# Kernel tuning notes

Hardware: AMD Instinct MI355X
Metric: run time of the kernel (lower is better)

Reference implementation:

```python
import jax, jax.numpy as jnp
import numpy as np

B, S, H, HD, WIN, KS = 2, 2048, 8, 64, 64, 2048
D = H * HD          # slotsize = nheads * headsize = 512
SUB = 1 + 2 * WIN   # window length = 129
LN_EPS = 1e-3       # Keras LayerNormalization default epsilon


def setup_inputs() -> dict:
    key = jax.random.key(0)
    ks = jax.random.split(key, 5)
    s = 0.02
    return {
        "values": jax.random.normal(ks[0], (B, S, D), jnp.float32),
        "W_kqv": jax.random.normal(ks[1], (D, 3 * D), jnp.float32) * s,
        "b_kqv": jnp.zeros((3 * D,), jnp.float32),
        "ln_gamma": jnp.ones((D,), jnp.float32),
        "ln_beta": jnp.zeros((D,), jnp.float32),
        "W_kernel": jax.random.normal(ks[2], (D, KS), jnp.float32) * s,
        "b_kernel": jnp.zeros((KS,), jnp.float32),
        "W_proj": jax.random.normal(ks[3], (KS, D), jnp.float32) * s,
        "b_proj": jnp.zeros((D,), jnp.float32),
    }


def _layernorm(x, g, b):
    mu = jnp.mean(x, axis=-1, keepdims=True)
    var = jnp.var(x, axis=-1, keepdims=True)
    return (x - mu) * jax.lax.rsqrt(var + LN_EPS) * g + b


def reference(values, W_kqv, b_kqv, ln_gamma, ln_beta, W_kernel, b_kernel, W_proj, b_proj):
    # fused qkv projection: [B,S,3D]
    kqv = values @ W_kqv + b_kqv
    k, q, v = jnp.split(kqv, 3, axis=2)
    # shared layernorm applied to q and k (over full D)
    q = _layernorm(q, ln_gamma, ln_beta)
    k = _layernorm(k, ln_gamma, ln_beta)
    kh = k.reshape(B, S, H, HD)
    qh = q.reshape(B, S, H, HD)
    vh = v.reshape(B, S, H, HD)
    starts = jnp.clip(jnp.arange(S) - WIN, 0, S - SUB)
    idx = starts[:, None] + jnp.arange(SUB)          # [S, SUB]
    kw = kh[:, idx]                                  # [B,S,SUB,H,HD]
    vw = vh[:, idx]                                  # [B,S,SUB,H,HD]
    scores = jnp.einsum('bshd,bswhd->bshw', qh, kw) / np.float32(np.sqrt(HD))
    attn = jax.nn.softmax(scores, axis=-1)           # [B,S,H,SUB]
    ctx = jnp.einsum('bshw,bswhd->bshd', attn, vw).reshape(B, S, D)
    # residual MLP (dropout rate 0 -> identity)
    x = jax.nn.relu(ctx @ W_kernel + b_kernel)
    x = x @ W_proj + b_proj
    return x + v  # residual is the value projection, per the original code
```

## Files before the change

### kernel.cpp

```cpp
#include <hip/hip_runtime.h>
#include <hip/hip_bf16.h>

#define B_ 2
#define S_ 2048
#define H_ 8
#define HD_ 64
#define WIN_ 64
#define SUB_ 129
#define D_ 512
#define KS_ 2048
#define M_ 4096
#define LN_EPS 1e-3f

typedef unsigned short u16;
typedef short bf16x8 __attribute__((ext_vector_type(8)));
typedef _Float16 f16x8 __attribute__((ext_vector_type(8)));
typedef float f32x4 __attribute__((ext_vector_type(4)));

__device__ inline u16 f2bf(float x) {
  unsigned int u = __float_as_uint(x);
  return (u16)((u + 0x7fffu + ((u >> 16) & 1u)) >> 16);
}

__device__ inline void gll16(const u16* g, u16* l) {
  __builtin_amdgcn_global_load_lds(
      (const __attribute__((address_space(1))) void*)g,
      (__attribute__((address_space(3))) void*)l, 16, 0, 0);
}

template <int EPI>
__global__ __launch_bounds__(256) void mfma_gemm(
    const u16* __restrict__ A, const u16* __restrict__ Bt,
    const float* __restrict__ bias, const float* __restrict__ extra,
    void* __restrict__ Cout, int K, int lda, int ldb, int ldc, int eld,
    int TN) {
  __shared__ __align__(16) u16 As[2][8192];
  __shared__ __align__(16) u16 Bs[2][8192];

  const int tid = threadIdx.x;
  const int wv = tid >> 6;
  const int ln = tid & 63;

  const int id = blockIdx.x;
  const int xcd = id & 7;
  const int sub = id >> 3;
  const int tn = sub % TN;
  const int msub = sub / TN;
  const int row0 = (xcd * 4 + msub) << 7;
  const int col0 = tn << 7;

  const int lrow = ln >> 3;
  const int lchunk = (ln & 7) ^ lrow;
  const u16* ag = A + (size_t)(row0 + 32 * wv + lrow) * lda + lchunk * 8;
  const u16* bg = Bt + (size_t)(col0 + 32 * wv + lrow) * ldb + lchunk * 8;
  const int lbase = 32 * wv * 64;

  const int q = ln >> 4;
  const int r16 = ln & 15;
  const int r8 = r16 & 7;
  const int wm = (wv & 1) << 6;
  const int wn = (wv >> 1) << 6;

  f32x4 acc[4][4];
#pragma unroll
  for (int i = 0; i < 4; ++i)
#pragma unroll
    for (int j = 0; j < 4; ++j) acc[i][j] = (f32x4){0.f, 0.f, 0.f, 0.f};

#define STAGE(buf, koff)                                            \
  do {                                                              \
    const u16* a0 = ag + (koff);                                    \
    const u16* b0 = bg + (koff);                                    \
    u16* la = &As[buf][lbase];                                      \
    u16* lb = &Bs[buf][lbase];                                      \
    gll16(a0, la);                                                  \
    gll16(a0 + 8 * (size_t)lda, la + 512);                          \
    gll16(a0 + 16 * (size_t)lda, la + 1024);                        \
    gll16(a0 + 24 * (size_t)lda, la + 1536);                        \
    gll16(b0, lb);                                                  \
    gll16(b0 + 8 * (size_t)ldb, lb + 512);                          \
    gll16(b0 + 16 * (size_t)ldb, lb + 1024);                        \
    gll16(b0 + 24 * (size_t)ldb, lb + 1536);                        \
  } while (0)

  const int nk = K >> 6;
  STAGE(0, 0);

  for (int ki = 0; ki < nk; ++ki) {
    __syncthreads();
    if (ki + 1 < nk) STAGE((ki + 1) & 1, (ki + 1) << 6);

    const char* Ab = (const char*)As[ki & 1];
    const char* Bb = (const char*)Bs[ki & 1];
#pragma unroll
    for (int ks = 0; ks < 2; ++ks) {
      const int pc = ((q + 4 * ks) ^ r8) << 4;
      bf16x8 af[4], bfv[4];
#pragma unroll
      for (int mi = 0; mi < 4; ++mi)
        af[mi] = *(const bf16x8*)(Ab + (wm + 16 * mi + r16) * 128 + pc);
#pragma unroll
      for (int ni = 0; ni < 4; ++ni)
        bfv[ni] = *(const bf16x8*)(Bb + (wn + 16 * ni + r16) * 128 + pc);
#pragma unroll
      for (int mi = 0; mi < 4; ++mi)
#pragma unroll
        for (int ni = 0; ni < 4; ++ni)
          acc[mi][ni] = __builtin_amdgcn_mfma_f32_16x16x32_bf16(
              af[mi], bfv[ni], acc[mi][ni], 0, 0, 0);
    }
  }
#undef STAGE

  const int colb = col0 + wn + r16;
  float bv[4];
#pragma unroll
  for (int ni = 0; ni < 4; ++ni) bv[ni] = bias[colb + ni * 16];

#pragma unroll
  for (int mi = 0; mi < 4; ++mi) {
#pragma unroll
    for (int ni = 0; ni < 4; ++ni) {
      const int col = colb + ni * 16;
#pragma unroll
      for (int r = 0; r < 4; ++r) {
        const int row = row0 + wm + mi * 16 + (q << 2) + r;
        float v = acc[mi][ni][r] + bv[ni];
        if (EPI == 0) {
          ((float*)Cout)[(size_t)row * ldc + col] = v;
        } else if (EPI == 1) {
          ((u16*)Cout)[(size_t)row * ldc + col] = f2bf(fmaxf(v, 0.f));
        } else {
          ((float*)Cout)[(size_t)row * ldc + col] =
              v + extra[(size_t)row * eld + col];
        }
      }
    }
  }
}

__global__ __launch_bounds__(256) void cvt_kernel(const float* __restrict__ in,
                                                  u16* __restrict__ out) {
  const int i = (blockIdx.x * 256 + threadIdx.x) * 8;
  float4 a = *(const float4*)&in[i];
  float4 b = *(const float4*)&in[i + 4];
  union { u16 u[8]; uint4 v; } pk;
  pk.u[0] = f2bf(a.x); pk.u[1] = f2bf(a.y); pk.u[2] = f2bf(a.z); pk.u[3] = f2bf(a.w);
  pk.u[4] = f2bf(b.x); pk.u[5] = f2bf(b.y); pk.u[6] = f2bf(b.z); pk.u[7] = f2bf(b.w);
  *(uint4*)&out[i] = pk.v;
}

__global__ __launch_bounds__(256) void cvtT_kernel(const float* __restrict__ W,
                                                   u16* __restrict__ Wt, int K,
                                                   int N) {
  __shared__ float t[32][33];
  const int n0 = blockIdx.x << 5;
  const int k0 = blockIdx.y << 5;
  const int r = threadIdx.x >> 3;
  const int c4 = (threadIdx.x & 7) << 2;
  float4 v = *(const float4*)&W[(size_t)(k0 + r) * N + n0 + c4];
  t[r][c4 + 0] = v.x; t[r][c4 + 1] = v.y; t[r][c4 + 2] = v.z; t[r][c4 + 3] = v.w;
  __syncthreads();
  ushort4 o;
  o.x = f2bf(t[c4 + 0][r]); o.y = f2bf(t[c4 + 1][r]);
  o.z = f2bf(t[c4 + 2][r]); o.w = f2bf(t[c4 + 3][r]);
  *(ushort4*)&Wt[(size_t)(n0 + r) * K + k0 + c4] = o;
}

__global__ __launch_bounds__(128) void ln_kernel(float* __restrict__ kqv,
                                                 const float* __restrict__ gamma,
                                                 const float* __restrict__ beta) {
  const int row = blockIdx.x;
  const int bs = row >> 1;
  const int which = row & 1;
  float* p = kqv + (size_t)bs * 1536 + (which ? 512 : 0);
  const int tid = threadIdx.x;
  const int c = tid << 2;

  float4 xv = *(float4*)&p[c];
  float s = xv.x + xv.y + xv.z + xv.w;
  float ss = xv.x * xv.x + xv.y * xv.y + xv.z * xv.z + xv.w * xv.w;

#pragma unroll
  for (int off = 32; off > 0; off >>= 1) {
    s += __shfl_down(s, off);
    ss += __shfl_down(ss, off);
  }
  __shared__ float red[4];
  if ((tid & 63) == 0) {
    red[(tid >> 6) * 2 + 0] = s;
    red[(tid >> 6) * 2 + 1] = ss;
  }
  __syncthreads();
  const float tot = red[0] + red[2];
  const float tots = red[1] + red[3];
  const float mean = tot * (1.f / 512.f);
  const float var = tots * (1.f / 512.f) - mean * mean;
  const float rstd = rsqrtf(var + LN_EPS);

  float4 g = *(const float4*)&gamma[c];
  float4 bb = *(const float4*)&beta[c];
  xv.x = (xv.x - mean) * rstd * g.x + bb.x;
  xv.y = (xv.y - mean) * rstd * g.y + bb.y;
  xv.z = (xv.z - mean) * rstd * g.z + bb.z;
  xv.w = (xv.w - mean) * rstd * g.w + bb.w;
  *(float4*)&p[c] = xv;
}

__global__ __launch_bounds__(256) void attn_kernel(const float* __restrict__ kqv,
                                                   u16* __restrict__ ctx) {
  __shared__ __align__(16) u16 Ks[192 * 64];
  __shared__ __align__(16) u16 Vt[64 * 192];
  __shared__ __align__(16) u16 Ps[4 * 16 * 192];

  const int bid = blockIdx.x;
  const int tile = bid & 31;
  const int h = (bid >> 5) & 7;
  const int b = bid >> 8;
  const int t0 = tile << 6;

  int g0 = t0 - WIN_;
  if (g0 < 0) g0 = 0;
  if (g0 > S_ - SUB_) g0 = S_ - SUB_;

  const int tid = threadIdx.x;
  const size_t rowb = (size_t)(b * S_);

#pragma unroll
  for (int it = 0; it < 6; ++it) {
    const int item = tid + it * 256;
    const int key = item >> 3, c = item & 7;
    const int phys = c ^ (key & 7);
    const float* kp = &kqv[(rowb + g0 + key) * 1536 + h * 64 + c * 8];
    float4 a = *(const float4*)kp;
    float4 bb = *(const float4*)(kp + 4);
    union { u16 u[8]; uint4 v; } pk;
    pk.u[0] = f2bf(a.x); pk.u[1] = f2bf(a.y); pk.u[2] = f2bf(a.z); pk.u[3] = f2bf(a.w);
    pk.u[4] = f2bf(bb.x); pk.u[5] = f2bf(bb.y); pk.u[6] = f2bf(bb.z); pk.u[7] = f2bf(bb.w);
    *(uint4*)&Ks[key * 64 + phys * 8] = pk.v;
  }
#pragma unroll
  for (int it = 0; it < 2; ++it) {
    const int item = tid + it * 256;
    const int qq = item >> 3, c = item & 7;
    const int phys = c ^ (qq & 7);
    const float* qp = &kqv[(rowb + t0 + qq) * 1536 + 512 + h * 64 + c * 8];
    float4 a = *(const float4*)qp;
    float4 bb = *(const float4*)(qp + 4);
    union { u16 u[8]; uint4 v; } pk;
    pk.u[0] = f2bf(a.x * 0.125f); pk.u[1] = f2bf(a.y * 0.125f);
    pk.u[2] = f2bf(a.z * 0.125f); pk.u[3] = f2bf(a.w * 0.125f);
    pk.u[4] = f2bf(bb.x * 0.125f); pk.u[5] = f2bf(bb.y * 0.125f);
    pk.u[6] = f2bf(bb.z * 0.125f); pk.u[7] = f2bf(bb.w * 0.125f);
    *(uint4*)&Ps[qq * 64 + phys * 8] = pk.v;
  }
#pragma unroll
  for (int it = 0; it < 12; ++it) {
    const int item = tid + it * 256;
    const int dg = item / 192;
    const int key = item - dg * 192;
    const float* vp = &kqv[(rowb + g0 + key) * 1536 + 1024 + h * 64 + dg * 4];
    float4 v = *(const float4*)vp;
#pragma unroll
    for (int j = 0; j < 4; ++j) {
      const int d = dg * 4 + j;
      const int c = key >> 3;
      const int phys = (c & 24) | ((c ^ d) & 7);
      const float f = (j == 0) ? v.x : (j == 1) ? v.y : (j == 2) ? v.z : v.w;
      *(_Float16*)&Vt[d * 192 + phys * 8 + (key & 7)] = (_Float16)f;
    }
  }
  __syncthreads();

  const int wv = tid >> 6;
  const int ln = tid & 63;
  const int quad = ln >> 4;
  const int l15 = ln & 15;
  const int l7 = l15 & 7;
  const int qbase = wv << 4;

  bf16x8 qf[2];
#pragma unroll
  for (int ks = 0; ks < 2; ++ks) {
    const int phys = (ks * 4 + quad) ^ l7;
    qf[ks] = *(const bf16x8*)&Ps[(qbase + l15) * 64 + phys * 8];
  }

  f32x4 sacc[12];
#pragma unroll
  for (int nt = 0; nt < 12; ++nt) sacc[nt] = (f32x4){0.f, 0.f, 0.f, 0.f};
#pragma unroll
  for (int ks = 0; ks < 2; ++ks) {
    const int phys = (ks * 4 + quad) ^ l7;
#pragma unroll
    for (int nt = 0; nt < 12; ++nt) {
      bf16x8 kf = *(const bf16x8*)&Ks[(nt * 16 + l15) * 64 + phys * 8];
      sacc[nt] = __builtin_amdgcn_mfma_f32_16x16x32_bf16(qf[ks], kf, sacc[nt], 0, 0, 0);
    }
  }

  int off[4];
#pragma unroll
  for (int r = 0; r < 4; ++r) {
    const int qg = t0 + qbase + quad * 4 + r;
    int st = qg - WIN_;
    if (st < 0) st = 0;
    if (st > S_ - SUB_) st = S_ - SUB_;
    off[r] = st - g0;
  }

  float rmax[4] = {-1e30f, -1e30f, -1e30f, -1e30f};
#pragma unroll
  for (int nt = 0; nt < 12; ++nt) {
    const int n = nt * 16 + l15;
#pragma unroll
    for (int r = 0; r < 4; ++r) {
      const bool valid = (n >= off[r]) && (n < off[r] + SUB_);
      const float v = valid ? sacc[nt][r] : -1e30f;
      sacc[nt][r] = v;
      rmax[r] = fmaxf(rmax[r], v);
    }
  }
#pragma unroll
  for (int m = 1; m < 16; m <<= 1)
#pragma unroll
    for (int r = 0; r < 4; ++r) rmax[r] = fmaxf(rmax[r], __shfl_xor(rmax[r], m));

  float rsum[4] = {0.f, 0.f, 0.f, 0.f};
#pragma unroll
  for (int nt = 0; nt < 12; ++nt) {
#pragma unroll
    for (int r = 0; r < 4; ++r) {
      const float e = __expf(sacc[nt][r] - rmax[r]);
      sacc[nt][r] = e;
      rsum[r] += e;
    }
  }
#pragma unroll
  for (int m = 1; m < 16; m <<= 1)
#pragma unroll
    for (int r = 0; r < 4; ++r) rsum[r] += __shfl_xor(rsum[r], m);
  float inv[4];
#pragma unroll
  for (int r = 0; r < 4; ++r) inv[r] = 1.f / rsum[r];

  __syncthreads();

  u16* psw = &Ps[wv * 16 * 192];
#pragma unroll
  for (int nt = 0; nt < 12; ++nt) {
    const int n = nt * 16 + l15;
    const int c = n >> 3;
#pragma unroll
    for (int r = 0; r < 4; ++r) {
      const int m = quad * 4 + r;
      const int phys = (c & 24) | ((c ^ m) & 7);
      *(_Float16*)&psw[m * 192 + phys * 8 + (n & 7)] = (_Float16)sacc[nt][r];
    }
  }
  __syncthreads();

  f32x4 oacc[4];
#pragma unroll
  for (int nt = 0; nt < 4; ++nt) oacc[nt] = (f32x4){0.f, 0.f, 0.f, 0.f};
#pragma unroll
  for (int ks = 0; ks < 6; ++ks) {
    const int c = ks * 4 + quad;
    const int phys = (c & 24) | ((c ^ l7) & 7);
    f16x8 pf = *(const f16x8*)&psw[l15 * 192 + phys * 8];
#pragma unroll
    for (int nt = 0; nt < 4; ++nt) {
      f16x8 vf = *(const f16x8*)&Vt[(nt * 16 + l15) * 192 + phys * 8];
      oacc[nt] = __builtin_amdgcn_mfma_f32_16x16x32_f16(pf, vf, oacc[nt], 0, 0, 0);
    }
  }

#pragma unroll
  for (int nt = 0; nt < 4; ++nt) {
#pragma unroll
    for (int r = 0; r < 4; ++r) {
      const int row = t0 + qbase + quad * 4 + r;
      const int col = h * 64 + nt * 16 + l15;
      ctx[(rowb + row) * D_ + col] = f2bf(oacc[nt][r] * inv[r]);
    }
  }
}

extern "C" void kernel_launch(void* const* d_in, const int* in_sizes, int n_in,
                              void* d_out, int out_size, void* d_ws,
                              size_t ws_size, hipStream_t stream) {
  (void)in_sizes; (void)n_in; (void)out_size; (void)ws_size;
  const float* values   = (const float*)d_in[0];
  const float* W_kqv    = (const float*)d_in[1];
  const float* b_kqv    = (const float*)d_in[2];
  const float* ln_gamma = (const float*)d_in[3];
  const float* ln_beta  = (const float*)d_in[4];
  const float* W_kernel = (const float*)d_in[5];
  const float* b_kernel = (const float*)d_in[6];
  const float* W_proj   = (const float*)d_in[7];
  const float* b_proj   = (const float*)d_in[8];
  float* out = (float*)d_out;

  float* kqv     = (float*)d_ws;
  u16*   vals_bf = (u16*)(kqv + (size_t)M_ * 1536);
  u16*   ctx_bf  = vals_bf + (size_t)M_ * 512;
  u16*   x_bf    = ctx_bf + (size_t)M_ * 512;
  u16*   wkqv_t  = x_bf + (size_t)M_ * 2048;
  u16*   wker_t  = wkqv_t + (size_t)1536 * 512;
  u16*   wproj_t = wker_t + (size_t)2048 * 512;

  cvt_kernel<<<(M_ * 512) / 2048, 256, 0, stream>>>(values, vals_bf);
  cvtT_kernel<<<dim3(1536 / 32, 512 / 32), 256, 0, stream>>>(W_kqv, wkqv_t, 512, 1536);
  cvtT_kernel<<<dim3(2048 / 32, 512 / 32), 256, 0, stream>>>(W_kernel, wker_t, 512, 2048);
  cvtT_kernel<<<dim3(512 / 32, 2048 / 32), 256, 0, stream>>>(W_proj, wproj_t, 2048, 512);

  mfma_gemm<0><<<384, 256, 0, stream>>>(
      vals_bf, wkqv_t, b_kqv, nullptr, kqv, 512, 512, 512, 1536, 0, 12);

  ln_kernel<<<2 * M_, 128, 0, stream>>>(kqv, ln_gamma, ln_beta);

  attn_kernel<<<B_ * H_ * (S_ / 64), 256, 0, stream>>>(kqv, ctx_bf);

  mfma_gemm<1><<<512, 256, 0, stream>>>(
      ctx_bf, wker_t, b_kernel, nullptr, x_bf, 512, 512, 512, KS_, 0, 16);

  mfma_gemm<2><<<128, 256, 0, stream>>>(
      x_bf, wproj_t, b_proj, kqv + 1024, out, 2048, 2048, 2048, D_, 1536, 4);
}
```

Before: 174.7 us.

## Store kqv intermediate in bf16 and use 64-row tiles for final GEMM

The QKV projection now writes a bf16 intermediate instead of fp32. The layernorm and attention kernels read bf16 directly, which removes the in-kernel conversions, and the PV MFMA switches from fp16 to bf16 with the 1/8 scale moved onto the scores. A new 64-row-tile GEMM variant launches twice as many blocks (256 vs 128) for the final projection and reads the bf16 residual. The intent is to halve intermediate memory traffic and raise parallelism in the last GEMM. The cost is lower precision for the residual v and for the layernorm inputs.

```diff
diff --git a/kernel.cpp b/kernel.cpp
--- a/kernel.cpp
+++ b/kernel.cpp
@@ -14,13 +14,17 @@
 
 typedef unsigned short u16;
 typedef short bf16x8 __attribute__((ext_vector_type(8)));
-typedef _Float16 f16x8 __attribute__((ext_vector_type(8)));
 typedef float f32x4 __attribute__((ext_vector_type(4)));
 
 __device__ inline u16 f2bf(float x) {
   unsigned int u = __float_as_uint(x);
   return (u16)((u + 0x7fffu + ((u >> 16) & 1u)) >> 16);
 }
+__device__ inline float bf2f(u16 u) {
+  return __uint_as_float(((unsigned int)u) << 16);
+}
+__device__ inline float bf2f_lo(unsigned int u) { return __uint_as_float(u << 16); }
+__device__ inline float bf2f_hi(unsigned int u) { return __uint_as_float(u & 0xffff0000u); }
 
 __device__ inline void gll16(const u16* g, u16* l) {
   __builtin_amdgcn_global_load_lds(
@@ -31,9 +35,8 @@
 template <int EPI>
 __global__ __launch_bounds__(256) void mfma_gemm(
     const u16* __restrict__ A, const u16* __restrict__ Bt,
-    const float* __restrict__ bias, const float* __restrict__ extra,
-    void* __restrict__ Cout, int K, int lda, int ldb, int ldc, int eld,
-    int TN) {
+    const float* __restrict__ bias, u16* __restrict__ Cout, int K, int lda,
+    int ldb, int ldc, int TN) {
   __shared__ __align__(16) u16 As[2][8192];
   __shared__ __align__(16) u16 Bs[2][8192];
 
@@ -126,14 +129,107 @@
       for (int r = 0; r < 4; ++r) {
         const int row = row0 + wm + mi * 16 + (q << 2) + r;
         float v = acc[mi][ni][r] + bv[ni];
-        if (EPI == 0) {
-          ((float*)Cout)[(size_t)row * ldc + col] = v;
-        } else if (EPI == 1) {
-          ((u16*)Cout)[(size_t)row * ldc + col] = f2bf(fmaxf(v, 0.f));
-        } else {
-          ((float*)Cout)[(size_t)row * ldc + col] =
-              v + extra[(size_t)row * eld + col];
-        }
+        if (EPI == 1) v = fmaxf(v, 0.f);
+        Cout[(size_t)row * ldc + col] = f2bf(v);
+      }
+    }
+  }
+}
+
+__global__ __launch_bounds__(256) void mfma_gemm64(
+    const u16* __restrict__ A, const u16* __restrict__ Bt,
+    const float* __restrict__ bias, const u16* __restrict__ extra,
+    float* __restrict__ Cout, int K, int lda, int ldb, int ldc, int eld,
+    int TN, int MB) {
+  __shared__ __align__(16) u16 As[2][4096];
+  __shared__ __align__(16) u16 Bs[2][8192];
+
+  const int tid = threadIdx.x;
+  const int wv = tid >> 6;
+  const int ln = tid & 63;
+
+  const int id = blockIdx.x;
+  const int xcd = id & 7;
+  const int sub = id >> 3;
+  const int tn = sub % TN;
+  const int msub = sub / TN;
+  const int row0 = (xcd * MB + msub) << 6;
+  const int col0 = tn << 7;
+
+  const int lrow = ln >> 3;
+  const int lchunk = (ln & 7) ^ lrow;
+  const u16* ag = A + (size_t)(row0 + 16 * wv + lrow) * lda + lchunk * 8;
+  const u16* bg = Bt + (size_t)(col0 + 32 * wv + lrow) * ldb + lchunk * 8;
+
+  const int q = ln >> 4;
+  const int r16 = ln & 15;
+  const int r8 = r16 & 7;
+  const int wn = wv << 5;
+
+  f32x4 acc[4][2];
+#pragma unroll
+  for (int i = 0; i < 4; ++i)
+#pragma unroll
+    for (int j = 0; j < 2; ++j) acc[i][j] = (f32x4){0.f, 0.f, 0.f, 0.f};
+
+#define STAGE64(buf, koff)                                          \
+  do {                                                              \
+    const u16* a0 = ag + (koff);                                    \
+    const u16* b0 = bg + (koff);                                    \
+    u16* la = &As[buf][wv * 1024];                                  \
+    u16* lb = &Bs[buf][wv * 2048];                                  \
+    gll16(a0, la);                                                  \
+    gll16(a0 + 8 * (size_t)lda, la + 512);                          \
+    gll16(b0, lb);                                                  \
+    gll16(b0 + 8 * (size_t)ldb, lb + 512);                          \
+    gll16(b0 + 16 * (size_t)ldb, lb + 1024);                        \
+    gll16(b0 + 24 * (size_t)ldb, lb + 1536);                        \
+  } while (0)
+
+  const int nk = K >> 6;
+  STAGE64(0, 0);
+
+  for (int ki = 0; ki < nk; ++ki) {
+    __syncthreads();
+    if (ki + 1 < nk) STAGE64((ki + 1) & 1, (ki + 1) << 6);
+
+    const char* Ab = (const char*)As[ki & 1];
+    const char* Bb = (const char*)Bs[ki & 1];
+#pragma unroll
+    for (int ks = 0; ks < 2; ++ks) {
+      const int pc = ((q + 4 * ks) ^ r8) << 4;
+      bf16x8 af[4], bfv[2];
+#pragma unroll
+      for (int mi = 0; mi < 4; ++mi)
+        af[mi] = *(const bf16x8*)(Ab + (16 * mi + r16) * 128 + pc);
+#pragma unroll
+      for (int ni = 0; ni < 2; ++ni)
+        bfv[ni] = *(const bf16x8*)(Bb + (wn + 16 * ni + r16) * 128 + pc);
+#pragma unroll
+      for (int mi = 0; mi < 4; ++mi)
+#pragma unroll
+        for (int ni = 0; ni < 2; ++ni)
+          acc[mi][ni] = __builtin_amdgcn_mfma_f32_16x16x32_bf16(
+              af[mi], bfv[ni], acc[mi][ni], 0, 0, 0);
+    }
+  }
+#undef STAGE64
+
+  const int colb = col0 + wn + r16;
+  float bv[2];
+#pragma unroll
+  for (int ni = 0; ni < 2; ++ni) bv[ni] = bias[colb + ni * 16];
+
+#pragma unroll
+  for (int mi = 0; mi < 4; ++mi) {
+#pragma unroll
+    for (int ni = 0; ni < 2; ++ni) {
+      const int col = colb + ni * 16;
+#pragma unroll
+      for (int r = 0; r < 4; ++r) {
+        const int row = row0 + mi * 16 + (q << 2) + r;
+        Cout[(size_t)row * ldc + col] =
+            acc[mi][ni][r] + bv[ni] + bf2f(extra[(size_t)row * eld + col]);
       }
     }
   }
@@ -167,19 +263,21 @@
   *(ushort4*)&Wt[(size_t)(n0 + r) * K + k0 + c4] = o;
 }
 
-__global__ __launch_bounds__(128) void ln_kernel(float* __restrict__ kqv,
+__global__ __launch_bounds__(128) void ln_kernel(u16* __restrict__ kqv,
                                                  const float* __restrict__ gamma,
                                                  const float* __restrict__ beta) {
   const int row = blockIdx.x;
   const int bs = row >> 1;
   const int which = row & 1;
-  float* p = kqv + (size_t)bs * 1536 + (which ? 512 : 0);
+  u16* p = kqv + (size_t)bs * 1536 + (which ? 512 : 0);
   const int tid = threadIdx.x;
   const int c = tid << 2;
 
-  float4 xv = *(float4*)&p[c];
-  float s = xv.x + xv.y + xv.z + xv.w;
-  float ss = xv.x * xv.x + xv.y * xv.y + xv.z * xv.z + xv.w * xv.w;
+  uint2 raw = *(uint2*)&p[c];
+  float x0 = bf2f_lo(raw.x), x1 = bf2f_hi(raw.x);
+  float x2 = bf2f_lo(raw.y), x3 = bf2f_hi(raw.y);
+  float s = x0 + x1 + x2 + x3;
+  float ss = x0 * x0 + x1 * x1 + x2 * x2 + x3 * x3;
 
 #pragma unroll
   for (int off = 32; off > 0; off >>= 1) {
@@ -200,14 +298,15 @@
 
   float4 g = *(const float4*)&gamma[c];
   float4 bb = *(const float4*)&beta[c];
-  xv.x = (xv.x - mean) * rstd * g.x + bb.x;
-  xv.y = (xv.y - mean) * rstd * g.y + bb.y;
-  xv.z = (xv.z - mean) * rstd * g.z + bb.z;
-  xv.w = (xv.w - mean) * rstd * g.w + bb.w;
-  *(float4*)&p[c] = xv;
-}
-
-__global__ __launch_bounds__(256) void attn_kernel(const float* __restrict__ kqv,
+  union { u16 u[4]; uint2 v; } o;
+  o.u[0] = f2bf((x0 - mean) * rstd * g.x + bb.x);
+  o.u[1] = f2bf((x1 - mean) * rstd * g.y + bb.y);
+  o.u[2] = f2bf((x2 - mean) * rstd * g.z + bb.z);
+  o.u[3] = f2bf((x3 - mean) * rstd * g.w + bb.w);
+  *(uint2*)&p[c] = o.v;
+}
+
+__global__ __launch_bounds__(256) void attn_kernel(const u16* __restrict__ kqv,
                                                    u16* __restrict__ ctx) {
   __shared__ __align__(16) u16 Ks[192 * 64];
   __shared__ __align__(16) u16 Vt[64 * 192];
@@ -231,43 +330,31 @@
     const int item = tid + it * 256;
     const int key = item >> 3, c = item & 7;
     const int phys = c ^ (key & 7);
-    const float* kp = &kqv[(rowb + g0 + key) * 1536 + h * 64 + c * 8];
-    float4 a = *(const float4*)kp;
-    float4 bb = *(const float4*)(kp + 4);
-    union { u16 u[8]; uint4 v; } pk;
-    pk.u[0] = f2bf(a.x); pk.u[1] = f2bf(a.y); pk.u[2] = f2bf(a.z); pk.u[3] = f2bf(a.w);
-    pk.u[4] = f2bf(bb.x); pk.u[5] = f2bf(bb.y); pk.u[6] = f2bf(bb.z); pk.u[7] = f2bf(bb.w);
-    *(uint4*)&Ks[key * 64 + phys * 8] = pk.v;
+    uint4 v = *(const uint4*)&kqv[(rowb + g0 + key) * 1536 + h * 64 + c * 8];
+    *(uint4*)&Ks[key * 64 + phys * 8] = v;
   }
 #pragma unroll
   for (int it = 0; it < 2; ++it) {
     const int item = tid + it * 256;
     const int qq = item >> 3, c = item & 7;
     const int phys = c ^ (qq & 7);
-    const float* qp = &kqv[(rowb + t0 + qq) * 1536 + 512 + h * 64 + c * 8];
-    float4 a = *(const float4*)qp;
-    float4 bb = *(const float4*)(qp + 4);
-    union { u16 u[8]; uint4 v; } pk;
-    pk.u[0] = f2bf(a.x * 0.125f); pk.u[1] = f2bf(a.y * 0.125f);
-    pk.u[2] = f2bf(a.z * 0.125f); pk.u[3] = f2bf(a.w * 0.125f);
-    pk.u[4] = f2bf(bb.x * 0.125f); pk.u[5] = f2bf(bb.y * 0.125f);
-    pk.u[6] = f2bf(bb.z * 0.125f); pk.u[7] = f2bf(bb.w * 0.125f);
-    *(uint4*)&Ps[qq * 64 + phys * 8] = pk.v;
+    uint4 v = *(const uint4*)&kqv[(rowb + t0 + qq) * 1536 + 512 + h * 64 + c * 8];
+    *(uint4*)&Ps[qq * 64 + phys * 8] = v;
   }
 #pragma unroll
   for (int it = 0; it < 12; ++it) {
     const int item = tid + it * 256;
-    const int dg = item / 192;
+    const int dg = item >> 7 == 0 ? item / 192 : item / 192;
     const int key = item - dg * 192;
-    const float* vp = &kqv[(rowb + g0 + key) * 1536 + 1024 + h * 64 + dg * 4];
-    float4 v = *(const float4*)vp;
+    uint2 v = *(const uint2*)&kqv[(rowb + g0 + key) * 1536 + 1024 + h * 64 + dg * 4];
+    const int c = key >> 3;
+    u16 e[4] = {(u16)(v.x & 0xffff), (u16)(v.x >> 16),
+                (u16)(v.y & 0xffff), (u16)(v.y >> 16)};
 #pragma unroll
     for (int j = 0; j < 4; ++j) {
       const int d = dg * 4 + j;
-      const int c = key >> 3;
       const int phys = (c & 24) | ((c ^ d) & 7);
-      const float f = (j == 0) ? v.x : (j == 1) ? v.y : (j == 2) ? v.z : v.w;
-      *(_Float16*)&Vt[d * 192 + phys * 8 + (key & 7)] = (_Float16)f;
+      Vt[d * 192 + phys * 8 + (key & 7)] = e[j];
     }
   }
   __syncthreads();
@@ -316,7 +403,7 @@
 #pragma unroll
     for (int r = 0; r < 4; ++r) {
       const bool valid = (n >= off[r]) && (n < off[r] + SUB_);
-      const float v = valid ? sacc[nt][r] : -1e30f;
+      const float v = valid ? sacc[nt][r] * 0.125f : -1e30f;
       sacc[nt][r] = v;
       rmax[r] = fmaxf(rmax[r], v);
     }
@@ -355,7 +442,7 @@
     for (int r = 0; r < 4; ++r) {
       const int m = quad * 4 + r;
       const int phys = (c & 24) | ((c ^ m) & 7);
-      *(_Float16*)&psw[m * 192 + phys * 8 + (n & 7)] = (_Float16)sacc[nt][r];
+      psw[m * 192 + phys * 8 + (n & 7)] = f2bf(sacc[nt][r]);
     }
   }
   __syncthreads();
@@ -367,11 +454,11 @@
   for (int ks = 0; ks < 6; ++ks) {
     const int c = ks * 4 + quad;
     const int phys = (c & 24) | ((c ^ l7) & 7);
-    f16x8 pf = *(const f16x8*)&psw[l15 * 192 + phys * 8];
+    bf16x8 pf = *(const bf16x8*)&psw[l15 * 192 + phys * 8];
 #pragma unroll
     for (int nt = 0; nt < 4; ++nt) {
-      f16x8 vf = *(const f16x8*)&Vt[(nt * 16 + l15) * 192 + phys * 8];
-      oacc[nt] = __builtin_amdgcn_mfma_f32_16x16x32_f16(pf, vf, oacc[nt], 0, 0, 0);
+      bf16x8 vf = *(const bf16x8*)&Vt[(nt * 16 + l15) * 192 + phys * 8];
+      oacc[nt] = __builtin_amdgcn_mfma_f32_16x16x32_bf16(pf, vf, oacc[nt], 0, 0, 0);
     }
   }
 
@@ -401,29 +488,29 @@
   const float* b_proj   = (const float*)d_in[8];
   float* out = (float*)d_out;
 
-  float* kqv     = (float*)d_ws;
-  u16*   vals_bf = (u16*)(kqv + (size_t)M_ * 1536);
-  u16*   ctx_bf  = vals_bf + (size_t)M_ * 512;
-  u16*   x_bf    = ctx_bf + (size_t)M_ * 512;
-  u16*   wkqv_t  = x_bf + (size_t)M_ * 2048;
-  u16*   wker_t  = wkqv_t + (size_t)1536 * 512;
-  u16*   wproj_t = wker_t + (size_t)2048 * 512;
+  u16* kqv     = (u16*)d_ws;
+  u16* vals_bf = kqv + (size_t)M_ * 1536;
+  u16* ctx_bf  = vals_bf + (size_t)M_ * 512;
+  u16* x_bf    = ctx_bf + (size_t)M_ * 512;
+  u16* wkqv_t  = x_bf + (size_t)M_ * 2048;
+  u16* wker_t  = wkqv_t + (size_t)1536 * 512;
+  u16* wproj_t = wker_t + (size_t)2048 * 512;
 
   cvt_kernel<<<(M_ * 512) / 2048, 256, 0, stream>>>(values, vals_bf);
   cvtT_kernel<<<dim3(1536 / 32, 512 / 32), 256, 0, stream>>>(W_kqv, wkqv_t, 512, 1536);
   cvtT_kernel<<<dim3(2048 / 32, 512 / 32), 256, 0, stream>>>(W_kernel, wker_t, 512, 2048);
   cvtT_kernel<<<dim3(512 / 32, 2048 / 32), 256, 0, stream>>>(W_proj, wproj_t, 2048, 512);
 
-  mfma_gemm<0><<<384, 256, 0, stream>>>(
-      vals_bf, wkqv_t, b_kqv, nullptr, kqv, 512, 512, 512, 1536, 0, 12);
+  mfma_gemm<3><<<384, 256, 0, stream>>>(
+      vals_bf, wkqv_t, b_kqv, kqv, 512, 512, 512, 1536, 12);
 
   ln_kernel<<<2 * M_, 128, 0, stream>>>(kqv, ln_gamma, ln_beta);
 
   attn_kernel<<<B_ * H_ * (S_ / 64), 256, 0, stream>>>(kqv, ctx_bf);
 
   mfma_gemm<1><<<512, 256, 0, stream>>>(
-      ctx_bf, wker_t, b_kernel, nullptr, x_bf, 512, 512, 512, KS_, 0, 16);
-
-  mfma_gemm<2><<<128, 256, 0, stream>>>(
-      x_bf, wproj_t, b_proj, kqv + 1024, out, 2048, 2048, 2048, D_, 1536, 4);
-}
+      ctx_bf, wker_t, b_kernel, x_bf, 512, 512, 512, KS_, 16);
+
+  mfma_gemm64<<<256, 256, 0, stream>>>(
+      x_bf, wproj_t, b_proj, kqv + 1024, out, KS_, KS_, KS_, D_, 1536, 4, 8);
+}
```

Result: faster. 159.1 us (-8.9%).
